# Performance work log

Hardware: AMD Instinct MI355X
Metric: run time of the kernel (lower is better)

Reference implementation:

```python
import jax, jax.numpy as jnp
import numpy as np
from jax import lax

C = 256          # hidden_channels
K_ITERS = 3      # num_iterations

def _conv(x, w, b, stride=1, pad='SAME'):
    y = lax.conv_general_dilated(x, w, (stride, stride), pad,
                                 dimension_numbers=('NCHW', 'OIHW', 'NCHW'))
    return y + b[None, :, None, None]

def setup_inputs() -> dict:
    key = jax.random.key(0)
    ks = jax.random.split(key, 16)
    B, N, H, W = 1, 3, 384, 384
    def p(k, sh, scale=None):
        if scale is None:
            scale = 1.0 / np.sqrt(np.prod(sh[1:]))
        return jax.random.normal(k, sh, jnp.float32) * scale
    z = lambda: jnp.zeros((C,), jnp.float32)
    return {
        'frames': jax.random.normal(ks[0], (B, N, 3, H, W), jnp.float32),
        'backbone_w': p(ks[1], (C, 3, 8, 8)), 'backbone_b': z(),
        'W_intra': p(ks[2], (C, C), scale=1.0 / C),
        'W_inter': p(ks[3], (C, C), scale=1.0 / C),
        'gate_w': p(ks[4], (C, C, 1, 1)), 'gate_b': z(),
        'Wz': p(ks[5], (C, 2 * C, 3, 3)), 'bz': z(),
        'Wr': p(ks[6], (C, 2 * C, 3, 3)), 'br': z(),
        'Wh': p(ks[7], (C, 2 * C, 3, 3)), 'bh': z(),
        'ro_w1': p(ks[8], (C, 2 * C, 3, 3)), 'ro_b1': z(),
        'ro_w2': p(ks[9], (1, C, 3, 3)), 'ro_b2': jnp.zeros((1,), jnp.float32),
    }

def _forward(frames, backbone_w, backbone_b, W_intra, W_inter, gate_w, gate_b,
             Wz, bz, Wr, br, Wh, bh, ro_w1, ro_b1, ro_w2, ro_b2):
    B, N, _, H, W = frames.shape
    x = frames.reshape(B * N, 3, H, W)
    # backbone: stride-8 conv + ReLU -> node embeddings v (B*N, C, Hf, Wf)
    v = jax.nn.relu(_conv(x, backbone_w, backbone_b, stride=8, pad='VALID'))
    Hf, Wf = v.shape[2], v.shape[3]
    P = Hf * Wf
    v = v.reshape(B, N, C, Hf, Wf)
    h = v
    idx = jnp.arange(N)
    for _ in range(K_ITERS):
        hp = h.reshape(B, N, C, P).transpose(0, 1, 3, 2)      # (B,N,P,C)
        # inter attention e_ij = h_i W h_j^T over all ordered pairs
        t = jnp.einsum('bipc,cd->bipd', hp, W_inter)
        e = jnp.einsum('bipd,bjqd->bijpq', t, hp)              # (B,N,N,P,P)
        # intra (loop-edge) attention on the diagonal, own weight
        ti = jnp.einsum('bipc,cd->bipd', hp, W_intra)
        e_intra = jnp.einsum('bipd,biqd->bipq', ti, hp)        # (B,N,P,P)
        e = e.at[:, idx, idx].set(e_intra)
        attn = jax.nn.softmax(e, axis=-1)
        m = jnp.einsum('bijpq,bjqc->bijpc', attn, hp)          # msg j->i (B,N,N,P,C)
        m = m.transpose(0, 1, 2, 4, 3).reshape(B * N * N, C, Hf, Wf)
        # gated aggregation: sigmoid(1x1 conv) gate, sum over senders j
        g = jax.nn.sigmoid(_conv(m, gate_w, gate_b))
        magg = (g * m).reshape(B, N, N, C, Hf, Wf).sum(axis=2).reshape(B * N, C, Hf, Wf)
        # ConvGRU update
        hflat = h.reshape(B * N, C, Hf, Wf)
        mh = jnp.concatenate([magg, hflat], axis=1)
        zg = jax.nn.sigmoid(_conv(mh, Wz, bz))
        rg = jax.nn.sigmoid(_conv(mh, Wr, br))
        hc = jnp.tanh(_conv(jnp.concatenate([magg, rg * hflat], axis=1), Wh, bh))
        h = ((1.0 - zg) * hflat + zg * hc).reshape(B, N, C, Hf, Wf)
    # read-out on concat(h, v)
    cat = jnp.concatenate([h, v], axis=2).reshape(B * N, 2 * C, Hf, Wf)
    y = jax.nn.relu(_conv(cat, ro_w1, ro_b1))
    masks = _conv(y, ro_w2, ro_b2)
    return masks.reshape(B, N, 1, Hf, Wf)

def reference(frames, backbone_w, backbone_b, W_intra, W_inter, gate_w, gate_b,
              Wz, bz, Wr, br, Wh, bh, ro_w1, ro_b1, ro_w2, ro_b2):
    return _forward(frames, backbone_w, backbone_b, W_intra, W_inter, gate_w, gate_b,
                    Wz, bz, Wr, br, Wh, bh, ro_w1, ro_b1, ro_w2, ro_b2)
```

## Files before the change

### kernel.cpp

```cpp
#include <hip/hip_runtime.h>
#include <hip/hip_bf16.h>
#include <math.h>

#define PIX 2304
#define CCH 256
#define CP  589824
#define NCP 1769472
#define KC  4608
#define PADR 2512

typedef __hip_bfloat16 bf16;
typedef __attribute__((ext_vector_type(8))) short bf16x8;
typedef __attribute__((ext_vector_type(4))) float f32x4;

__device__ __forceinline__ float sigmoidf_(float x){ return 1.f/(1.f+__expf(-x)); }

__device__ __forceinline__ void gl_lds16(const bf16* g, bf16* lds){
    __builtin_amdgcn_global_load_lds(
        (const __attribute__((address_space(1))) void*)g,
        (__attribute__((address_space(3))) void*)lds, 16, 0, 0);
}
#define FENCE() asm volatile("" ::: "memory")

__device__ __forceinline__ float bperm_f(int srcLane, float v){
    return __int_as_float(__builtin_amdgcn_ds_bpermute(srcLane<<2, __float_as_int(v)));
}
__device__ __forceinline__ unsigned packbf(float lo, float hi){
    bf16 a = __float2bfloat16(lo), b = __float2bfloat16(hi);
    return (unsigned)(*(unsigned short*)&a) | ((unsigned)(*(unsigned short*)&b)<<16);
}

__global__ __launch_bounds__(384) void fattn_k(
    const bf16* __restrict__ T, const bf16* __restrict__ Ti,
    const bf16* __restrict__ Khp, const bf16* __restrict__ Vcp,
    bf16* __restrict__ Ob)
{
    __shared__ bf16 Ks[2][64*256];
    __shared__ bf16 Vs[2][256*64];
    __shared__ unsigned Ps[6][512];
    const int z = blockIdx.z, i = z/3, j = z%3;
    const bf16* Q  = ((i==j)? Ti : T) + (long)i*CP;
    const bf16* Kp = Khp + (long)j*CP;
    const bf16* Vp = Vcp + (long)j*CP;
    const int tid = threadIdx.x, l = tid & 63, w = tid >> 6;
    const int g = l>>4, m = l&15;
    const int q0 = blockIdx.x*96;

    bf16x8 qf[8];
    {
        const bf16* qr = Q + (long)(q0 + w*16 + m)*256 + g*8;
        #pragma unroll
        for (int ks=0; ks<8; ++ks) qf[ks] = *(const bf16x8*)(qr + ks*32);
    }
    f32x4 oacc[16];
    #pragma unroll
    for (int nf=0; nf<16; ++nf) oacc[nf] = (f32x4){0.f,0.f,0.f,0.f};
    float mrun = -3e38f;
    float lrun = 0.f;

    auto stage = [&](int buf, int t){
        const int kq = t*64;
        #pragma unroll
        for (int u=0; u<6; ++u){
            int idx = u*384 + tid;
            if (idx < 2048){
                int rr = idx>>5, cc = idx&31;
                gl_lds16(Kp + (long)(kq+rr)*256 + ((cc ^ (rr&7))<<3),
                         &Ks[buf][(u*384 + (tid & ~63))*8]);
            }
        }
        #pragma unroll
        for (int u=0; u<6; ++u){
            int idx = u*384 + tid;
            if (idx < 2048){
                int rr = idx>>3, cc = idx&7;
                gl_lds16(Vp + (long)rr*2304 + kq + ((cc ^ (rr&7))<<3),
                         &Vs[buf][(u*384 + (tid & ~63))*8]);
            }
        }
    };

    stage(0, 0);
    int cur = 0;
    char* pw = (char*)&Ps[w][0];
    for (int t=0; t<36; ++t){
        if (t+1 < 36){
            stage(cur^1, t+1);
            asm volatile("s_waitcnt vmcnt(10)" ::: "memory");
        } else {
            asm volatile("s_waitcnt vmcnt(0)" ::: "memory");
        }
        __builtin_amdgcn_s_barrier();
        FENCE();

        f32x4 sacc[4];
        #pragma unroll
        for (int nf=0; nf<4; ++nf) sacc[nf] = (f32x4){0.f,0.f,0.f,0.f};
        __builtin_amdgcn_s_setprio(1);
        #pragma unroll
        for (int ks=0; ks<8; ++ks){
            #pragma unroll
            for (int nf=0; nf<4; ++nf){
                int row = nf*16 + m;
                int phys = (ks*4 + g) ^ (row&7);
                bf16x8 kf = *(const bf16x8*)&Ks[cur][row*256 + phys*8];
                sacc[nf] = __builtin_amdgcn_mfma_f32_16x16x32_bf16(kf, qf[ks], sacc[nf], 0,0,0);
            }
        }
        __builtin_amdgcn_s_setprio(0);

        float pmax = -3e38f;
        #pragma unroll
        for (int nf=0; nf<4; ++nf)
            #pragma unroll
            for (int r=0; r<4; ++r) pmax = fmaxf(pmax, sacc[nf][r]);
        pmax = fmaxf(pmax, __shfl_xor(pmax, 16));
        pmax = fmaxf(pmax, __shfl_xor(pmax, 32));
        if (!__all(pmax - mrun <= 8.f)){
            float mn = fmaxf(mrun, pmax);
            float al = __expf(mrun - mn);
            mrun = mn;
            lrun *= al;
            float ar[4];
            #pragma unroll
            for (int r=0; r<4; ++r) ar[r] = bperm_f((l & 48) | (g*4 + r), al);
            #pragma unroll
            for (int nf=0; nf<16; ++nf)
                #pragma unroll
                for (int r=0; r<4; ++r) oacc[nf][r] *= ar[r];
        }
        float rs = 0.f;
        unsigned pk[4][2];
        #pragma unroll
        for (int nf=0; nf<4; ++nf){
            float p0 = __expf(sacc[nf][0] - mrun);
            float p1 = __expf(sacc[nf][1] - mrun);
            float p2 = __expf(sacc[nf][2] - mrun);
            float p3 = __expf(sacc[nf][3] - mrun);
            rs += (p0+p1) + (p2+p3);
            pk[nf][0] = packbf(p0, p1);
            pk[nf][1] = packbf(p2, p3);
        }
        rs += __shfl_xor(rs, 16);
        rs += __shfl_xor(rs, 32);
        lrun += rs;
        #pragma unroll
        for (int nf=0; nf<4; ++nf)
            #pragma unroll
            for (int s=0; s<2; ++s){
                int ba = m*128 + ((nf*32 + g*8 + s*4) ^ ((m&7)<<4));
                *(unsigned*)(pw + ba) = pk[nf][s];
            }
        asm volatile("s_waitcnt lgkmcnt(0)" ::: "memory");
        __builtin_amdgcn_sched_barrier(0);
        __builtin_amdgcn_s_setprio(1);
        #pragma unroll
        for (int ks2=0; ks2<2; ++ks2){
            bf16x8 pa = *(const bf16x8*)(pw + m*128 + ((ks2*64 + g*16) ^ ((m&7)<<4)));
            #pragma unroll
            for (int nf=0; nf<16; ++nf){
                int row = nf*16 + m;
                int phys = (ks2*4 + g) ^ (row&7);
                bf16x8 bv = *(const bf16x8*)&Vs[cur][row*64 + phys*8];
                oacc[nf] = __builtin_amdgcn_mfma_f32_16x16x32_bf16(pa, bv, oacc[nf], 0,0,0);
            }
        }
        __builtin_amdgcn_s_setprio(0);
        FENCE();
        __builtin_amdgcn_s_barrier();
        FENCE();
        cur ^= 1;
    }

    float linv = 1.f / lrun;
    float li[4];
    #pragma unroll
    for (int r=0; r<4; ++r) li[r] = bperm_f((l & 48) | (g*4 + r), linv);
    bf16* ob = Ob + (long)z*CP;
    const int prow0 = q0 + w*16 + g*4;
    #pragma unroll
    for (int nf=0; nf<16; ++nf){
        int c = nf*16 + m;
        #pragma unroll
        for (int r=0; r<4; ++r)
            ob[(long)(prow0+r)*256 + c] = __float2bfloat16(oacc[nf][r]*li[r]);
    }
}

template<int BN>
__global__ __launch_bounds__(256) void mgemm_k(
    const bf16* __restrict__ A0, const bf16* __restrict__ B, bf16* __restrict__ ob,
    int M, int lda, int ldb, int ldc,
    long bsB, long bsC, int nzJ, int Ksub)
{
    __shared__ bf16 As[2][128*64];
    __shared__ bf16 Bs[2][BN*64];
    const int jz = blockIdx.z % nzJ;
    const bf16* Ap = A0 + (long)blockIdx.x*128*lda;
    const bf16* Bp = B + jz*bsB + (long)blockIdx.y*BN*ldb;
    const int tid = threadIdx.x, l = tid & 63;
    const int wvu = tid & ~63;
    const int wr = tid>>7, wc = (tid>>6)&1;
    constexpr int NF = BN/32;
    f32x4 acc[4][NF];
    #pragma unroll
    for (int i=0;i<4;++i)
        #pragma unroll
        for (int j=0;j<NF;++j) acc[i][j] = (f32x4){0.f,0.f,0.f,0.f};

    auto stage = [&](int buf, int kb){
        #pragma unroll
        for (int u=0;u<4;++u){
            int idx = u*256 + tid;
            int row = idx>>3, g = (idx&7) ^ (row&7);
            gl_lds16(Ap + (long)row*lda + kb + g*8, &As[buf][(u*256+wvu)*8]);
        }
        #pragma unroll
        for (int u=0;u<BN/32;++u){
            int idx = u*256 + tid;
            int row = idx>>3, g = (idx&7) ^ (row&7);
            gl_lds16(Bp + (long)row*ldb + kb + g*8, &Bs[buf][(u*256+wvu)*8]);
        }
    };

    const int nk = Ksub >> 6;
    stage(0, 0);
    int cur = 0;
    for (int t=0; t<nk; ++t){
        if (t+1 < nk){
            stage(cur^1, (t+1)*64);
            if constexpr (BN==64) asm volatile("s_waitcnt vmcnt(6)" ::: "memory");
            else                  asm volatile("s_waitcnt vmcnt(8)" ::: "memory");
        } else {
            asm volatile("s_waitcnt vmcnt(0)" ::: "memory");
        }
        __builtin_amdgcn_s_barrier();
        FENCE();
        #pragma unroll
        for (int ks=0; ks<64; ks+=32){
            bf16x8 af[4], bfr[NF];
            #pragma unroll
            for (int i=0;i<4;++i){
                int row = wr*64 + i*16 + (l&15);
                af[i] = *(const bf16x8*)&As[cur][row*64 + ((((ks>>3)+(l>>4)) ^ (row&7))<<3)];
            }
            #pragma unroll
            for (int j=0;j<NF;++j){
                int row = wc*(BN/2) + j*16 + (l&15);
                bfr[j] = *(const bf16x8*)&Bs[cur][row*64 + ((((ks>>3)+(l>>4)) ^ (row&7))<<3)];
            }
            #pragma unroll
            for (int i=0;i<4;++i)
                #pragma unroll
                for (int j=0;j<NF;++j)
                    acc[i][j] = __builtin_amdgcn_mfma_f32_16x16x32_bf16(af[i], bfr[j], acc[i][j], 0,0,0);
        }
        FENCE();
        __builtin_amdgcn_s_barrier();
        FENCE();
        cur ^= 1;
    }

    const int mb = blockIdx.x*128 + wr*64, nb = blockIdx.y*BN + wc*(BN/2);
    #pragma unroll
    for (int i=0;i<4;++i)
        #pragma unroll
        for (int j=0;j<NF;++j){
            int gm0 = mb + i*16 + ((l>>4)<<2);
            int gn  = nb + j*16 + (l&15);
            #pragma unroll
            for (int r=0;r<4;++r)
                ob[jz*bsC + (long)(gm0+r)*ldc + gn] = __float2bfloat16(acc[i][j][r]);
        }
}

__global__ __launch_bounds__(256) void gatemm_k(
    const bf16* __restrict__ gatew, const bf16* __restrict__ Mb9,
    const float* __restrict__ gb, bf16* __restrict__ inpad)
{
    __shared__ bf16 As[2][128*64];
    __shared__ bf16 Bs[2][64*64];
    __shared__ bf16 Ts[64*136];
    const int tid = threadIdx.x, l = tid & 63, wvu = tid & ~63;
    const int wr = tid>>7, wc = (tid>>6)&1;
    const int i = blockIdx.z;
    const bf16* Ap = gatew + (long)blockIdx.x*128*256;
    const int nb0 = blockIdx.y*64;
    f32x4 msum[4][2];
    #pragma unroll
    for (int a=0;a<4;++a){ msum[a][0]=(f32x4){0,0,0,0}; msum[a][1]=(f32x4){0,0,0,0}; }

    for (int j=0; j<3; ++j){
        const bf16* Bp = Mb9 + (long)(i*3+j)*CP + (long)nb0*256;
        f32x4 acc[4][2];
        #pragma unroll
        for (int a=0;a<4;++a){ acc[a][0]=(f32x4){0,0,0,0}; acc[a][1]=(f32x4){0,0,0,0}; }
        auto stage = [&](int buf, int kb){
            #pragma unroll
            for (int u=0;u<4;++u){
                int idx = u*256 + tid;
                int row = idx>>3, g = (idx&7) ^ (row&7);
                gl_lds16(Ap + (long)row*256 + kb + g*8, &As[buf][(u*256+wvu)*8]);
            }
            #pragma unroll
            for (int u=0;u<2;++u){
                int idx = u*256 + tid;
                int row = idx>>3, g = (idx&7) ^ (row&7);
                gl_lds16(Bp + (long)row*256 + kb + g*8, &Bs[buf][(u*256+wvu)*8]);
            }
        };
        stage(0, 0);
        int cur = 0;
        for (int t=0; t<4; ++t){
            if (t+1 < 4){
                stage(cur^1, (t+1)*64);
                asm volatile("s_waitcnt vmcnt(6)" ::: "memory");
            } else {
                asm volatile("s_waitcnt vmcnt(0)" ::: "memory");
            }
            __builtin_amdgcn_s_barrier();
            FENCE();
            #pragma unroll
            for (int ks=0; ks<64; ks+=32){
                bf16x8 af[4], bfr[2];
                #pragma unroll
                for (int a=0;a<4;++a){
                    int row = wr*64 + a*16 + (l&15);
                    af[a] = *(const bf16x8*)&As[cur][row*64 + ((((ks>>3)+(l>>4)) ^ (row&7))<<3)];
                }
                #pragma unroll
                for (int b=0;b<2;++b){
                    int row = wc*32 + b*16 + (l&15);
                    bfr[b] = *(const bf16x8*)&Bs[cur][row*64 + ((((ks>>3)+(l>>4)) ^ (row&7))<<3)];
                }
                #pragma unroll
                for (int a=0;a<4;++a)
                    #pragma unroll
                    for (int b=0;b<2;++b)
                        acc[a][b] = __builtin_amdgcn_mfma_f32_16x16x32_bf16(af[a], bfr[b], acc[a][b], 0,0,0);
            }
            FENCE();
            __builtin_amdgcn_s_barrier();
            FENCE();
            cur ^= 1;
        }
        const bf16* mbz = Mb9 + (long)(i*3+j)*CP;
        const int mb = blockIdx.x*128 + wr*64;
        #pragma unroll
        for (int a=0;a<4;++a)
            #pragma unroll
            for (int b=0;b<2;++b){
                int gm0 = mb + a*16 + ((l>>4)<<2);
                int gn  = nb0 + wc*32 + b*16 + (l&15);
                #pragma unroll
                for (int r=0;r<4;++r){
                    int gm = gm0 + r;
                    float g = sigmoidf_(acc[a][b][r] + gb[gm]);
                    float mv = __bfloat162float(mbz[(long)gn*256 + gm]);
                    msum[a][b][r] += g*mv;
                }
            }
    }
    __syncthreads();
    const int mbl = wr*64;
    #pragma unroll
    for (int a=0;a<4;++a)
        #pragma unroll
        for (int b=0;b<2;++b){
            int cl0 = mbl + a*16 + ((l>>4)<<2);
            int pl  = wc*32 + b*16 + (l&15);
            #pragma unroll
            for (int r=0;r<4;++r)
                Ts[pl*136 + cl0 + r] = __float2bfloat16(msum[a][b][r]);
        }
    __syncthreads();
    const int pl = tid >> 2, seg = tid & 3;
    int p = nb0 + pl;
    int prow = p + 2*(p/48) + 51;
    bf16* dst = inpad + (long)i*PADR*512 + (long)prow*512 + blockIdx.x*128 + seg*32;
    #pragma unroll
    for (int k2=0; k2<4; ++k2)
        *(uint4*)(dst + k2*8) = *(const uint4*)&Ts[pl*136 + seg*32 + k2*8];
}

__global__ __launch_bounds__(256) void cgemm2_k(
    const bf16* __restrict__ inpad, const bf16* __restrict__ W,
    float* __restrict__ part, int N)
{
    __shared__ bf16 As[2][128*64];
    __shared__ bf16 Bs[2][128*64];
    const int tid = threadIdx.x, l = tid & 63, wvu = tid & ~63;
    const int wr = tid>>7, wc = (tid>>6)&1;
    const int bx = blockIdx.x, by = blockIdx.y, kc = blockIdx.z;
    const int img = bx/18, m0 = (bx - img*18)*128;
    const bf16* Ab = inpad + (long)img*PADR*512;
    const bf16* Bb = W + (long)by*128*KC;
    f32x4 acc[4][4];
    #pragma unroll
    for (int i=0;i<4;++i)
        #pragma unroll
        for (int j=0;j<4;++j) acc[i][j] = (f32x4){0.f,0.f,0.f,0.f};

    auto stageA = [&](int buf, int k0){
        int tap = k0 >> 9, ci0 = k0 & 511;
        int dy = tap/3, dx = tap - 3*dy;
        int shift = (dy-1)*50 + (dx-1);
        #pragma unroll
        for (int u=0;u<4;++u){
            int idx = u*256 + tid;
            int row = idx>>3;
            int om = m0 + row;
            int prow = om + 2*(om/48) + 51 + shift;
            int g = (idx&7) ^ (row&7);
            gl_lds16(Ab + (long)prow*512 + ci0 + g*8, &As[buf][(u*256+wvu)*8]);
        }
    };
    auto stageB = [&](int buf, int k0){
        #pragma unroll
        for (int u=0;u<4;++u){
            int idx = u*256 + tid;
            int row = idx>>3;
            int g = (idx&7) ^ (row&7);
            gl_lds16(Bb + (long)row*KC + k0 + g*8, &Bs[buf][(u*256+wvu)*8]);
        }
    };

    const int kbeg = kc*2304;
    stageA(0, kbeg); stageB(0, kbeg);
    int cur = 0;
    for (int t=0; t<36; ++t){
        if (t+1 < 36){
            stageA(cur^1, kbeg+(t+1)*64); stageB(cur^1, kbeg+(t+1)*64);
            asm volatile("s_waitcnt vmcnt(8)" ::: "memory");
        } else {
            asm volatile("s_waitcnt vmcnt(0)" ::: "memory");
        }
        __builtin_amdgcn_s_barrier();
        FENCE();
        #pragma unroll
        for (int ks=0; ks<64; ks+=32){
            bf16x8 af[4], bfr[4];
            #pragma unroll
            for (int i=0;i<4;++i){
                int row = wr*64 + i*16 + (l&15);
                af[i] = *(const bf16x8*)&As[cur][row*64 + ((((ks>>3)+(l>>4)) ^ (row&7))<<3)];
            }
            #pragma unroll
            for (int j=0;j<4;++j){
                int row = wc*64 + j*16 + (l&15);
                bfr[j] = *(const bf16x8*)&Bs[cur][row*64 + ((((ks>>3)+(l>>4)) ^ (row&7))<<3)];
            }
            #pragma unroll
            for (int i=0;i<4;++i)
                #pragma unroll
                for (int j=0;j<4;++j)
                    acc[i][j] = __builtin_amdgcn_mfma_f32_16x16x32_bf16(af[i], bfr[j], acc[i][j], 0,0,0);
        }
        FENCE();
        __builtin_amdgcn_s_barrier();
        FENCE();
        cur ^= 1;
    }

    float* pbase = part + (long)kc*N*6912 + (long)img*2304;
    #pragma unroll
    for (int i=0;i<4;++i)
        #pragma unroll
        for (int j=0;j<4;++j){
            int gm0 = m0 + wr*64 + i*16 + ((l>>4)<<2);
            int gn  = by*128 + wc*64 + j*16 + (l&15);
            *(f32x4*)&pbase[(long)gn*6912 + gm0] = acc[i][j];
        }
}

__global__ __launch_bounds__(256) void credzr_k(const float* __restrict__ part,
        const float* __restrict__ bz, const float* __restrict__ br,
        const float* __restrict__ h, float* __restrict__ zg, bf16* __restrict__ inpad)
{
    __shared__ float tz[64][65];
    const int img = blockIdx.z, p0 = blockIdx.x*64, c0 = blockIdx.y*64;
    const int t = threadIdx.x, tx = t&63, tq = t>>6;
    #pragma unroll
    for (int u=0;u<16;++u){
        int cl = tq + u*4, c = c0 + cl;
        long pz = (long)c*6912 + (long)img*2304 + p0 + tx;
        float vz = part[pz] + part[pz + 512L*6912];
        long pr = (long)(c+256)*6912 + (long)img*2304 + p0 + tx;
        float vr = part[pr] + part[pr + 512L*6912];
        long hidx = (long)img*CP + (long)c*PIX + p0 + tx;
        float hv = h[hidx];
        zg[hidx] = sigmoidf_(vz + bz[c]);
        tz[cl][tx] = sigmoidf_(vr + br[c]) * hv;
    }
    __syncthreads();
    #pragma unroll
    for (int u=0;u<16;++u){
        int pl = tq + u*4, p = p0 + pl;
        int prow = p + 2*(p/48) + 51;
        inpad[(long)img*PADR*512 + (long)prow*512 + 256 + c0 + tx] = __float2bfloat16(tz[tx][pl]);
    }
}

__global__ __launch_bounds__(256) void credht_k(const float* __restrict__ part,
        const float* __restrict__ bh, const float* __restrict__ zg,
        float* __restrict__ h, bf16* __restrict__ hcp, bf16* __restrict__ hp,
        bf16* __restrict__ inpad)
{
    __shared__ float th[64][65];
    const int img = blockIdx.z, p0 = blockIdx.x*64, c0 = blockIdx.y*64;
    const int t = threadIdx.x, tx = t&63, tq = t>>6;
    #pragma unroll
    for (int u=0;u<16;++u){
        int cl = tq + u*4, c = c0 + cl;
        long pidx = (long)c*6912 + (long)img*2304 + p0 + tx;
        float vv = part[pidx] + part[pidx + 256L*6912];
        float hc = tanhf(vv + bh[c]);
        long hidx = (long)img*CP + (long)c*PIX + p0 + tx;
        float zv = zg[hidx];
        float hn = (1.f - zv)*h[hidx] + zv*hc;
        h[hidx] = hn;
        hcp[hidx] = __float2bfloat16(hn);
        th[cl][tx] = hn;
    }
    __syncthreads();
    #pragma unroll
    for (int u=0;u<16;++u){
        int pl = tq + u*4, p = p0 + pl;
        float val = th[tx][pl];
        hp[(long)img*CP + (long)p*256 + c0 + tx] = __float2bfloat16(val);
        int prow = p + 2*(p/48) + 51;
        inpad[(long)img*PADR*512 + (long)prow*512 + 256 + c0 + tx] = __float2bfloat16(val);
    }
}

__global__ __launch_bounds__(256) void credro_k(const float* __restrict__ part,
        const float* __restrict__ b0, float* __restrict__ o0)
{
    int id = blockIdx.x*256 + threadIdx.x;
    int c = id / 6912, g = id - c*6912;
    int img = g / 2304, p = g - img*2304;
    float v = part[id] + part[id + 256L*6912];
    o0[(long)img*CP + (long)c*PIX + p] = fmaxf(v + b0[c], 0.f);
}

__global__ __launch_bounds__(256) void padtr_k(const float* __restrict__ src,
        bf16* __restrict__ dst, int cofs)
{
    __shared__ float tile[64][65];
    const int img = blockIdx.z, p0 = blockIdx.x*64, c0 = blockIdx.y*64;
    const int t = threadIdx.x, tx = t&63, tq = t>>6;
    #pragma unroll
    for (int u=0;u<16;++u){
        int r = tq + u*4;
        tile[r][tx] = src[(long)img*CP + (long)(c0+r)*PIX + p0 + tx];
    }
    __syncthreads();
    bf16* d = dst + (long)img*PADR*512 + cofs + c0;
    #pragma unroll
    for (int u=0;u<16;++u){
        int pl = tq + u*4;
        int p = p0 + pl;
        int prow = p + 2*(p/48) + 51;
        d[(long)prow*512 + tx] = __float2bfloat16(tile[tx][pl]);
    }
}

__global__ __launch_bounds__(256) void convw_k(const float* __restrict__ src,
        bf16* __restrict__ dst, int total)
{
    int idx = blockIdx.x*256 + threadIdx.x;
    if (idx >= total) return;
    int co = idx / KC, r = idx - co*KC;
    int tap = r >> 9, ci = r & 511;
    dst[idx] = __float2bfloat16(src[(long)co*KC + ci*9 + tap]);
}

__global__ __launch_bounds__(256) void prep_h_k(const float* __restrict__ h,
        bf16* __restrict__ hcp, bf16* __restrict__ hp)
{
    __shared__ float tile[64][65];
    const int i = blockIdx.z, p0 = blockIdx.x*64, c0 = blockIdx.y*64;
    const int t = threadIdx.x, tx = t&63, tq = t>>6;
    #pragma unroll
    for (int s=0;s<16;++s){
        int r = tq + s*4;
        float v = h[(long)i*CP + (long)(c0+r)*PIX + p0 + tx];
        tile[r][tx] = v;
        hcp[(long)i*CP + (long)(c0+r)*PIX + p0 + tx] = __float2bfloat16(v);
    }
    __syncthreads();
    #pragma unroll
    for (int s=0;s<16;++s){
        int r = tq + s*4;
        hp[(long)i*CP + (long)(p0+r)*256 + c0 + tx] = __float2bfloat16(tile[tx][r]);
    }
}

__global__ __launch_bounds__(256) void convert_w_k(const float* __restrict__ wint,
    const float* __restrict__ wintra, const float* __restrict__ gw, bf16* __restrict__ o)
{
    int t = blockIdx.x*256 + threadIdx.x;
    int d = t >> 8, c = t & 255;
    o[t]          = __float2bfloat16(wint[c*256 + d]);
    o[65536 + t]  = __float2bfloat16(wintra[c*256 + d]);
    o[131072 + t] = __float2bfloat16(gw[t]);
}

__global__ __launch_bounds__(256) void backbone_k(
    const float* __restrict__ frames, const float* __restrict__ W,
    const float* __restrict__ bias, float* __restrict__ v, float* __restrict__ h)
{
    __shared__ float wl[3*64*4];
    const int n = blockIdx.z, o0 = blockIdx.y * 4;
    const int p = blockIdx.x * 256 + threadIdx.x;
    const int y = p / 48, x = p % 48;
    for (int e = threadIdx.x; e < 768; e += 256) {
        int o_sel = e / 192, rem = e % 192, ci = rem / 64, k = rem % 64;
        wl[(ci*64 + k)*4 + o_sel] = W[((long)(o0 + o_sel)*3 + ci)*64 + k];
    }
    __syncthreads();
    float acc[4] = {0.f,0.f,0.f,0.f};
    for (int ci = 0; ci < 3; ++ci) {
        const float* src = frames + (((long)n*3 + ci)*384) * 384;
        #pragma unroll
        for (int k = 0; k < 64; ++k) {
            int ky = k >> 3, kx = k & 7;
            float iv = src[(8*y + ky)*384 + 8*x + kx];
            float4 w = ((const float4*)wl)[ci*64 + k];
            acc[0] += iv*w.x; acc[1] += iv*w.y; acc[2] += iv*w.z; acc[3] += iv*w.w;
        }
    }
    #pragma unroll
    for (int oo = 0; oo < 4; ++oo) {
        float r = fmaxf(acc[oo] + bias[o0 + oo], 0.f);
        long idx = ((long)n*CCH + o0 + oo)*PIX + p;
        v[idx] = r; h[idx] = r;
    }
}

__global__ __launch_bounds__(256) void maskpart_k(const float* __restrict__ yin,
        const float* __restrict__ W, float* __restrict__ part)
{
    __shared__ float wl[288];
    const int cb = blockIdx.y * 32;
    for (int e = threadIdx.x; e < 288; e += 256) wl[e] = W[cb*9 + e];
    __syncthreads();
    int id = blockIdx.x*256 + threadIdx.x;
    int n = id / PIX, p = id - n*PIX;
    int y = p / 48, x = p % 48;
    float acc = 0.f;
    for (int ci = 0; ci < 32; ++ci) {
        const float* src = yin + ((long)n*CCH + cb + ci)*PIX;
        #pragma unroll
        for (int dy = 0; dy < 3; ++dy) {
            int yy = y + dy - 1;
            #pragma unroll
            for (int dx = 0; dx < 3; ++dx) {
                int xx = x + dx - 1;
                float iv = (yy >= 0 && yy < 48 && xx >= 0 && xx < 48) ? src[yy*48 + xx] : 0.f;
                acc += iv * wl[ci*9 + dy*3 + dx];
            }
        }
    }
    part[(long)blockIdx.y*(3*PIX) + id] = acc;
}

__global__ __launch_bounds__(256) void maskred_k(const float* __restrict__ part,
        const float* __restrict__ bias, float* __restrict__ out)
{
    int id = blockIdx.x*256 + threadIdx.x;
    float acc = bias[0];
    #pragma unroll
    for (int s = 0; s < 8; ++s) acc += part[(long)s*(3*PIX) + id];
    out[id] = acc;
}

extern "C" void kernel_launch(void* const* d_in, const int* in_sizes, int n_in,
                              void* d_out, int out_size, void* d_ws, size_t ws_size,
                              hipStream_t stream)
{
    const float* frames     = (const float*)d_in[0];
    const float* backbone_w = (const float*)d_in[1];
    const float* backbone_b = (const float*)d_in[2];
    const float* W_intra    = (const float*)d_in[3];
    const float* W_inter    = (const float*)d_in[4];
    const float* gate_w     = (const float*)d_in[5];
    const float* gate_b     = (const float*)d_in[6];
    const float* Wz         = (const float*)d_in[7];
    const float* bz         = (const float*)d_in[8];
    const float* Wr         = (const float*)d_in[9];
    const float* br         = (const float*)d_in[10];
    const float* Wh         = (const float*)d_in[11];
    const float* bh         = (const float*)d_in[12];
    const float* ro_w1      = (const float*)d_in[13];
    const float* ro_b1      = (const float*)d_in[14];
    const float* ro_w2      = (const float*)d_in[15];
    const float* ro_b2      = (const float*)d_in[16];
    float* out = (float*)d_out;
    float* ws  = (float*)d_ws;

    float* h    = ws + 0L*NCP;
    float* v    = ws + 1L*NCP;
    float* zg   = ws + 3L*NCP;
    float* S    = ws + 7L*NCP;

    float* Mb9f   = S;
    float* hp16f  = S + 7962624;
    float* hcp16f = hp16f + 884736;
    float* t16f   = hcp16f + 884736;
    float* ti16f  = t16f + 884736;
    float* wbase  = S + 11501568;
    bf16* Wint_t   = (bf16*)wbase;
    bf16* Wintra_t = Wint_t + 65536;
    bf16* gatew16  = Wint_t + 131072;
    bf16* cw16     = (bf16*)(wbase + 98304);
    bf16* inpad    = (bf16*)(wbase + 98304 + 2359296);
    float* maskp   = wbase + 98304 + 2359296 + 1929216;

    bf16* Mb9    = (bf16*)Mb9f;
    bf16* hp16   = (bf16*)hp16f;
    bf16* hcp16  = (bf16*)hcp16f;
    bf16* t16    = (bf16*)t16f;
    bf16* ti16   = (bf16*)ti16f;
    float* cpart = Mb9f;

    dim3 b256(256);

    hipMemsetAsync(inpad, 0, 3858432*sizeof(bf16), stream);
    backbone_k<<<dim3(9,64,3), b256, 0, stream>>>(frames, backbone_w, backbone_b, v, h);
    convert_w_k<<<dim3(256), b256, 0, stream>>>(W_inter, W_intra, gate_w, Wint_t);
    convw_k<<<dim3(4608), b256, 0, stream>>>(Wz, cw16, 256*KC);
    convw_k<<<dim3(4608), b256, 0, stream>>>(Wr, cw16 + 256L*KC, 256*KC);
    convw_k<<<dim3(4608), b256, 0, stream>>>(Wh, cw16 + 512L*KC, 256*KC);
    convw_k<<<dim3(4608), b256, 0, stream>>>(ro_w1, cw16 + 768L*KC, 256*KC);

    prep_h_k<<<dim3(36,4,3), b256, 0, stream>>>(h, hcp16, hp16);
    padtr_k<<<dim3(36,4,3), b256, 0, stream>>>(h, inpad, 256);

    for (int it = 0; it < 3; ++it) {
        mgemm_k<64><<<dim3(54,4,2), b256, 0, stream>>>(hp16, Wint_t, t16,
            6912, 256,256,256, 65536L, 1769472L, 2, 256);
        fattn_k<<<dim3(24,1,9), dim3(384), 0, stream>>>(t16, ti16, hp16, hcp16, Mb9);
        gatemm_k<<<dim3(2,36,3), b256, 0, stream>>>(gatew16, Mb9, gate_b, inpad);
        cgemm2_k<<<dim3(54,4,2), b256, 0, stream>>>(inpad, cw16, cpart, 512);
        credzr_k<<<dim3(36,4,3), b256, 0, stream>>>(cpart, bz, br, h, zg, inpad);
        cgemm2_k<<<dim3(54,2,2), b256, 0, stream>>>(inpad, cw16 + 512L*KC, cpart, 256);
        credht_k<<<dim3(36,4,3), b256, 0, stream>>>(cpart, bh, zg, h, hcp16, hp16, inpad);
    }

    padtr_k<<<dim3(36,4,3), b256, 0, stream>>>(h, inpad, 0);
    padtr_k<<<dim3(36,4,3), b256, 0, stream>>>(v, inpad, 256);
    cgemm2_k<<<dim3(54,2,2), b256, 0, stream>>>(inpad, cw16 + 768L*KC, cpart, 256);
    credro_k<<<dim3(6912), b256, 0, stream>>>(cpart, ro_b1, zg);
    maskpart_k<<<dim3(27,8), b256, 0, stream>>>(zg, ro_w2, maskp);
    maskred_k<<<dim3(27), b256, 0, stream>>>(maskp, ro_b2, out);
}
```

Before: 859.7 us.

## Use 128-key KV tiles with split single-buffered K/V staging in flash attention

Doubles the attention key tile from 64 to 128, which halves the loop trip count and the barriers per key. The double-buffered K/V LDS tiles become single buffers. The next K tile is loaded while softmax and P·V run, and the next V tile is loaded while the next Q·K runs, with extra barriers and vmcnt waits to order these phases. This aims to cut per-iteration overhead and raise MFMA work per synchronization, but it uses more LDS and registers (eight score fragments) and overlaps loads less deeply than true double buffering.

```diff
diff --git a/kernel.cpp b/kernel.cpp
--- a/kernel.cpp
+++ b/kernel.cpp
@@ -35,9 +35,9 @@
     const bf16* __restrict__ Khp, const bf16* __restrict__ Vcp,
     bf16* __restrict__ Ob)
 {
-    __shared__ bf16 Ks[2][64*256];
-    __shared__ bf16 Vs[2][256*64];
-    __shared__ unsigned Ps[6][512];
+    __shared__ bf16 Ks[128*256];
+    __shared__ bf16 Vs[256*128];
+    __shared__ unsigned Ps[6][1024];
     const int z = blockIdx.z, i = z/3, j = z%3;
     const bf16* Q  = ((i==j)? Ti : T) + (long)i*CP;
     const bf16* Kp = Khp + (long)j*CP;
@@ -58,60 +58,61 @@
     float mrun = -3e38f;
     float lrun = 0.f;
 
-    auto stage = [&](int buf, int t){
-        const int kq = t*64;
-        #pragma unroll
-        for (int u=0; u<6; ++u){
+    auto stageK = [&](int t){
+        const int kq = t*128;
+        #pragma unroll
+        for (int u=0; u<11; ++u){
             int idx = u*384 + tid;
-            if (idx < 2048){
+            if (idx < 4096){
                 int rr = idx>>5, cc = idx&31;
                 gl_lds16(Kp + (long)(kq+rr)*256 + ((cc ^ (rr&7))<<3),
-                         &Ks[buf][(u*384 + (tid & ~63))*8]);
-            }
-        }
-        #pragma unroll
-        for (int u=0; u<6; ++u){
+                         &Ks[(u*384 + (tid & ~63))*8]);
+            }
+        }
+    };
+    auto stageV = [&](int t){
+        const int kq = t*128;
+        #pragma unroll
+        for (int u=0; u<11; ++u){
             int idx = u*384 + tid;
-            if (idx < 2048){
-                int rr = idx>>3, cc = idx&7;
+            if (idx < 4096){
+                int rr = idx>>4, cc = idx&15;
                 gl_lds16(Vp + (long)rr*2304 + kq + ((cc ^ (rr&7))<<3),
-                         &Vs[buf][(u*384 + (tid & ~63))*8]);
+                         &Vs[(u*384 + (tid & ~63))*8]);
             }
         }
     };
 
-    stage(0, 0);
-    int cur = 0;
+    stageK(0); stageV(0);
     char* pw = (char*)&Ps[w][0];
-    for (int t=0; t<36; ++t){
-        if (t+1 < 36){
-            stage(cur^1, t+1);
-            asm volatile("s_waitcnt vmcnt(10)" ::: "memory");
-        } else {
-            asm volatile("s_waitcnt vmcnt(0)" ::: "memory");
-        }
+    for (int t=0; t<18; ++t){
+        asm volatile("s_waitcnt vmcnt(10)" ::: "memory");
         __builtin_amdgcn_s_barrier();
         FENCE();
 
-        f32x4 sacc[4];
-        #pragma unroll
-        for (int nf=0; nf<4; ++nf) sacc[nf] = (f32x4){0.f,0.f,0.f,0.f};
+        f32x4 sacc[8];
+        #pragma unroll
+        for (int nf=0; nf<8; ++nf) sacc[nf] = (f32x4){0.f,0.f,0.f,0.f};
         __builtin_amdgcn_s_setprio(1);
         #pragma unroll
         for (int ks=0; ks<8; ++ks){
             #pragma unroll
-            for (int nf=0; nf<4; ++nf){
+            for (int nf=0; nf<8; ++nf){
                 int row = nf*16 + m;
                 int phys = (ks*4 + g) ^ (row&7);
-                bf16x8 kf = *(const bf16x8*)&Ks[cur][row*256 + phys*8];
+                bf16x8 kf = *(const bf16x8*)&Ks[row*256 + phys*8];
                 sacc[nf] = __builtin_amdgcn_mfma_f32_16x16x32_bf16(kf, qf[ks], sacc[nf], 0,0,0);
             }
         }
         __builtin_amdgcn_s_setprio(0);
+        FENCE();
+        __builtin_amdgcn_s_barrier();
+        FENCE();
+        if (t+1 < 18) stageK(t+1);
 
         float pmax = -3e38f;
         #pragma unroll
-        for (int nf=0; nf<4; ++nf)
+        for (int nf=0; nf<8; ++nf)
             #pragma unroll
             for (int r=0; r<4; ++r) pmax = fmaxf(pmax, sacc[nf][r]);
         pmax = fmaxf(pmax, __shfl_xor(pmax, 16));
@@ -130,9 +131,9 @@
                 for (int r=0; r<4; ++r) oacc[nf][r] *= ar[r];
         }
         float rs = 0.f;
-        unsigned pk[4][2];
-        #pragma unroll
-        for (int nf=0; nf<4; ++nf){
+        unsigned pk[8][2];
+        #pragma unroll
+        for (int nf=0; nf<8; ++nf){
             float p0 = __expf(sacc[nf][0] - mrun);
             float p1 = __expf(sacc[nf][1] - mrun);
             float p2 = __expf(sacc[nf][2] - mrun);
@@ -145,23 +146,29 @@
         rs += __shfl_xor(rs, 32);
         lrun += rs;
         #pragma unroll
-        for (int nf=0; nf<4; ++nf)
+        for (int nf=0; nf<8; ++nf)
             #pragma unroll
             for (int s=0; s<2; ++s){
-                int ba = m*128 + ((nf*32 + g*8 + s*4) ^ ((m&7)<<4));
+                int ba = m*256 + ((nf*32 + g*8 + s*4) ^ ((m&7)<<4));
                 *(unsigned*)(pw + ba) = pk[nf][s];
             }
         asm volatile("s_waitcnt lgkmcnt(0)" ::: "memory");
         __builtin_amdgcn_sched_barrier(0);
+
+        if (t+1 < 18) asm volatile("s_waitcnt vmcnt(10)" ::: "memory");
+        else          asm volatile("s_waitcnt vmcnt(0)"  ::: "memory");
+        __builtin_amdgcn_s_barrier();
+        FENCE();
+
         __builtin_amdgcn_s_setprio(1);
         #pragma unroll
-        for (int ks2=0; ks2<2; ++ks2){
-            bf16x8 pa = *(const bf16x8*)(pw + m*128 + ((ks2*64 + g*16) ^ ((m&7)<<4)));
+        for (int ks2=0; ks2<4; ++ks2){
+            bf16x8 pa = *(const bf16x8*)(pw + m*256 + ((ks2*64 + g*16) ^ ((m&7)<<4)));
             #pragma unroll
             for (int nf=0; nf<16; ++nf){
                 int row = nf*16 + m;
                 int phys = (ks2*4 + g) ^ (row&7);
-                bf16x8 bv = *(const bf16x8*)&Vs[cur][row*64 + phys*8];
+                bf16x8 bv = *(const bf16x8*)&Vs[row*128 + phys*8];
                 oacc[nf] = __builtin_amdgcn_mfma_f32_16x16x32_bf16(pa, bv, oacc[nf], 0,0,0);
             }
         }
@@ -169,7 +176,7 @@
         FENCE();
         __builtin_amdgcn_s_barrier();
         FENCE();
-        cur ^= 1;
+        if (t+1 < 18) stageV(t+1);
     }
 
     float linv = 1.f / lrun;
```

Result: no change. 844.0 us (-1.8%).
